# Optimization experiments

Measured on AMD Instinct MI355X. Metric: run time of the kernel, lower is better.

The kernel has to match this reference:

```python
import jax, jax.numpy as jnp
import numpy as np

# model dims (match init_kwargs)
D = 1024      # input_dim
H = 4096      # hidden_dim
O = 1024      # expert_output_dim
E = 8         # num_experts
K = 2         # top_k


def setup_inputs() -> dict:
    key = jax.random.key(0)
    ks = jax.random.split(key, 8)
    B, S = 2, 2048
    x = jax.random.normal(ks[0], (B, S, D), dtype=jnp.float32)
    s = 0.02
    Wr = jax.random.normal(ks[1], (D, E), dtype=jnp.float32) * s
    br = jnp.zeros((E,), dtype=jnp.float32)
    W1 = jax.random.normal(ks[2], (E, D, H), dtype=jnp.float32) * s
    b1 = jnp.zeros((E, H), dtype=jnp.float32)
    W2 = jax.random.normal(ks[3], (E, H, O), dtype=jnp.float32) * s
    b2 = jnp.zeros((E, O), dtype=jnp.float32)
    return {"x": x, "Wr": Wr, "br": br, "W1": W1, "b1": b1, "W2": W2, "b2": b2}


def reference(x, Wr, br, W1, b1, W2, b2):
    B, S, _ = x.shape
    T = B * S
    xf = x.reshape(T, D)                                  # [T, D]
    logits = xf @ Wr + br                                 # [T, E]
    topk_logits, topk_idx = jax.lax.top_k(logits, K)      # [T, K]
    gates = jax.nn.softmax(topk_logits, axis=1)           # softmax over the K selected logits
    # scatter gates into a dense [T, E] matrix (top-k indices are unique per token)
    dense_gates = jnp.zeros((T, E), dtype=logits.dtype).at[
        jnp.arange(T)[:, None], topk_idx
    ].set(gates)
    # run every expert FFN densely, then combine with (mostly-zero) gates
    h = jax.nn.relu(jnp.einsum('td,edh->teh', xf, W1) + b1)   # [T, E, H]
    y = jnp.einsum('teh,eho->teo', h, W2) + b2                # [T, E, O]
    out = jnp.einsum('te,teo->to', dense_gates, y)            # [T, O]
    return out.reshape(B, S, O)
```

## Files before the change

### kernel.cpp

```cpp
#include <hip/hip_runtime.h>
#include <stdint.h>

#define KD 1024
#define KH 4096
#define KO 1024
#define KE 8
#define KT 4096

typedef unsigned short u16;
typedef __bf16 bf16x8 __attribute__((ext_vector_type(8)));
typedef unsigned short ushort8 __attribute__((ext_vector_type(8)));
typedef float floatx4 __attribute__((ext_vector_type(4)));

__device__ __forceinline__ u16 f2bf(float f) {
  unsigned u = __float_as_uint(f);
  u += 0x7fffu + ((u >> 16) & 1u);
  return (u16)(u >> 16);
}

__device__ __forceinline__ void glds16(const u16* g, u16* l) {
  __builtin_amdgcn_global_load_lds(
      (const __attribute__((address_space(1))) unsigned int*)(g),
      (__attribute__((address_space(3))) unsigned int*)(l), 16, 0, 0);
}

#define WAITV8 asm volatile("s_waitcnt vmcnt(8)" ::: "memory")
#define WAITV0 asm volatile("s_waitcnt vmcnt(0)" ::: "memory")
#define WAITLG asm volatile("s_waitcnt lgkmcnt(0)" ::: "memory")
#define BAR    __builtin_amdgcn_s_barrier()

__global__ void cvt_x_k(const float* __restrict__ x, u16* __restrict__ xbf) {
  int i = blockIdx.x * blockDim.x + threadIdx.x;
  float4 v = ((const float4*)x)[i];
  union { u16 u[4]; uint2 v2; } o;
  o.u[0] = f2bf(v.x); o.u[1] = f2bf(v.y); o.u[2] = f2bf(v.z); o.u[3] = f2bf(v.w);
  ((uint2*)xbf)[i] = o.v2;
}

__global__ __launch_bounds__(256) void transpose_k(const float* __restrict__ in,
                                                   u16* __restrict__ out, int R, int C) {
  __shared__ float tile[64][65];
  const int e = blockIdx.z;
  const float* I = in + (size_t)e * R * C;
  u16* Oo = out + (size_t)e * R * C;
  const int c0 = blockIdx.x * 64, r0 = blockIdx.y * 64;
  const int t = threadIdx.x;
  const int rr = t >> 4;
  const int c4 = (t & 15) << 2;
#pragma unroll
  for (int j = 0; j < 4; j++) {
    int r = rr + j * 16;
    float4 v = *(const float4*)&I[(size_t)(r0 + r) * C + c0 + c4];
    tile[r][c4] = v.x; tile[r][c4 + 1] = v.y; tile[r][c4 + 2] = v.z; tile[r][c4 + 3] = v.w;
  }
  __syncthreads();
  const int cc = t >> 3;
  const int rb = (t & 7) << 3;
#pragma unroll
  for (int j = 0; j < 2; j++) {
    int c = cc + j * 32;
    ushort8 o;
#pragma unroll
    for (int k = 0; k < 8; k++) o[k] = f2bf(tile[rb + k][c]);
    *(ushort8*)&Oo[(size_t)(c0 + c) * R + r0 + rb] = o;
  }
}

__global__ void router_k(const float* __restrict__ x, const float* __restrict__ Wr,
                         const float* __restrict__ br, int* __restrict__ eidx,
                         float2* __restrict__ gpair) {
  const int t = blockIdx.x;
  const int lane = threadIdx.x;
  const float* xr = x + (size_t)t * KD;
  double acc[KE];
#pragma unroll
  for (int e = 0; e < KE; e++) acc[e] = 0.0;
  for (int i = lane; i < KD; i += 64) {
    float xv = xr[i];
    const float* wr = Wr + i * KE;
#pragma unroll
    for (int e = 0; e < KE; e++) acc[e] += (double)xv * (double)wr[e];
  }
#pragma unroll
  for (int e = 0; e < KE; e++) {
#pragma unroll
    for (int m = 32; m > 0; m >>= 1) acc[e] += __shfl_xor(acc[e], m, 64);
  }
  if (lane == 0) {
    float l[KE];
#pragma unroll
    for (int e = 0; e < KE; e++) l[e] = (float)acc[e] + br[e];
    int i0 = 0;
#pragma unroll
    for (int e = 1; e < KE; e++) if (l[e] > l[i0]) i0 = e;
    int i1 = -1;
#pragma unroll
    for (int e = 0; e < KE; e++) {
      if (e == i0) continue;
      if (i1 < 0 || l[e] > l[i1]) i1 = e;
    }
    float g0 = 1.0f / (1.0f + expf(l[i1] - l[i0]));
    eidx[t] = i0 | (i1 << 4);
    gpair[t] = make_float2(g0, 1.0f - g0);
  }
}

__global__ __launch_bounds__(256) void bucket_k(const int* __restrict__ eidx,
                                                int* __restrict__ cnt,
                                                int* __restrict__ tok,
                                                int* __restrict__ pos) {
  const int e = blockIdx.x;
  const int tid = threadIdx.x;
  const int t0 = tid * 16;
  int f[16]; int c = 0;
#pragma unroll
  for (int j = 0; j < 16; j++) {
    int pk = eidx[t0 + j];
    int h0 = ((pk & 15) == e);
    int h1 = (((pk >> 4) & 15) == e);
    f[j] = h0 ? 1 : (h1 ? 2 : 0);
    c += (f[j] != 0);
  }
  __shared__ int sc[256];
  sc[tid] = c;
  __syncthreads();
  for (int d = 1; d < 256; d <<= 1) {
    int add = (tid >= d) ? sc[tid - d] : 0;
    __syncthreads();
    sc[tid] += add;
    __syncthreads();
  }
  int base = sc[tid] - c;
  if (tid == 0) cnt[e] = sc[255];
#pragma unroll
  for (int j = 0; j < 16; j++) {
    if (f[j]) {
      tok[(e << 12) + base] = t0 + j;
      pos[2 * (t0 + j) + (f[j] - 1)] = base;
      base++;
    }
  }
}

__global__ void offsets_k(const int* __restrict__ cnt, int* __restrict__ offs) {
  if (threadIdx.x == 0 && blockIdx.x == 0) {
    int s = 0;
#pragma unroll
    for (int e = 0; e < KE; e++) { offs[e] = s; s += cnt[e]; }
  }
}

__global__ __launch_bounds__(256) void gemm1_k(
    const u16* __restrict__ xbf, const u16* __restrict__ w1t,
    const float* __restrict__ b1, const int* __restrict__ cnt,
    const int* __restrict__ offs, const int* __restrict__ tok,
    u16* __restrict__ hbuf) {
  const int e = blockIdx.z;
  const int me = cnt[e];
  const int m0 = blockIdx.y * 128;
  if (m0 >= me) return;
  const int n0 = blockIdx.x * 128;
  const int oe = offs[e];
  const int* tk = tok + (e << 12);

  __shared__ u16 As[2 * 8192];
  __shared__ u16 Bs[2 * 8192];

  const int tid = threadIdx.x;
  const int lane = tid & 63;
  const int w = tid >> 6;
  const int wm = w >> 1, wn = w & 1;

  const int rr = lane >> 2;
  const int cc = (lane & 3) << 3;
  const int ar0 = m0 + w * 32 + rr;
  const int ar1 = ar0 + 16;
  const int ta0 = (ar0 < me) ? tk[ar0] : 0;
  const int ta1 = (ar1 < me) ? tk[ar1] : 0;
  const u16* ga0 = xbf + ((size_t)ta0 << 10) + cc;
  const u16* ga1 = xbf + ((size_t)ta1 << 10) + cc;
  const int br0 = n0 + w * 32 + rr;
  const u16* gb0 = w1t + ((size_t)e << 22) + ((size_t)br0 << 10) + cc;
  const u16* gb1 = gb0 + (16 << 10);
  u16* la00 = &As[w * 1024] + lane * 8;
  u16* lb00 = &Bs[w * 1024] + lane * 8;

  floatx4 acc[4][4] = {};
  const int fr = lane & 15;
  const int kq = (lane >> 4) << 3;

  auto stage = [&](int k64, int off) {
    glds16(ga0 + k64,      la00 + off);
    glds16(ga1 + k64,      la00 + off + 512);
    glds16(ga0 + k64 + 32, la00 + off + 4096);
    glds16(ga1 + k64 + 32, la00 + off + 4096 + 512);
    glds16(gb0 + k64,      lb00 + off);
    glds16(gb1 + k64,      lb00 + off + 512);
    glds16(gb0 + k64 + 32, lb00 + off + 4096);
    glds16(gb1 + k64 + 32, lb00 + off + 4096 + 512);
  };
  auto compute = [&](int off) {
#pragma unroll
    for (int p = 0; p < 2; p++) {
      bf16x8 af[4], bfr[4];
#pragma unroll
      for (int i = 0; i < 4; i++) {
        af[i]  = __builtin_bit_cast(bf16x8, *(const ushort8*)&As[off + p * 4096 + (wm * 64 + i * 16 + fr) * 32 + kq]);
        bfr[i] = __builtin_bit_cast(bf16x8, *(const ushort8*)&Bs[off + p * 4096 + (wn * 64 + i * 16 + fr) * 32 + kq]);
      }
#pragma unroll
      for (int mi = 0; mi < 4; mi++)
#pragma unroll
        for (int ni = 0; ni < 4; ni++)
          acc[mi][ni] = __builtin_amdgcn_mfma_f32_16x16x32_bf16(af[mi], bfr[ni], acc[mi][ni], 0, 0, 0);
    }
  };

  stage(0, 0);
  stage(64, 8192);
  for (int kt = 0; kt < KD / 64 - 2; kt += 2) {
    WAITV8; BAR; compute(0);    WAITLG; BAR; stage((kt + 2) * 64, 0);
    WAITV8; BAR; compute(8192); WAITLG; BAR; stage((kt + 3) * 64, 8192);
  }
  WAITV8; BAR; compute(0);
  WAITV0; BAR; compute(8192);

  const int q = lane >> 4;
#pragma unroll
  for (int ni = 0; ni < 4; ni++) {
    const int gcol = n0 + wn * 64 + ni * 16 + fr;
    const float bb = b1[(e << 12) + gcol];
#pragma unroll
    for (int mi = 0; mi < 4; mi++) {
#pragma unroll
      for (int r = 0; r < 4; r++) {
        const int gr = m0 + wm * 64 + mi * 16 + q * 4 + r;
        if (gr < me) {
          float v = fmaxf(acc[mi][ni][r] + bb, 0.0f);
          hbuf[((size_t)(oe + gr) << 12) + gcol] = f2bf(v);
        }
      }
    }
  }
}

__global__ __launch_bounds__(256) void gemm2_k(
    const u16* __restrict__ hbuf, const u16* __restrict__ w2t,
    const int* __restrict__ cnt, const int* __restrict__ offs,
    float* __restrict__ y) {
  const int e = blockIdx.z;
  const int me = cnt[e];
  const int m0 = blockIdx.y * 128;
  if (m0 >= me) return;
  const int ks = blockIdx.x & 1;
  const int n0 = (blockIdx.x >> 1) * 128;
  const int k0 = ks * (KH / 2);
  const int oe = offs[e];

  __shared__ u16 As[2 * 8192];
  __shared__ u16 Bs[2 * 8192];

  const int tid = threadIdx.x;
  const int lane = tid & 63;
  const int w = tid >> 6;
  const int wm = w >> 1, wn = w & 1;

  const int rr = lane >> 2;
  const int cc = (lane & 3) << 3;
  const int ar0 = m0 + w * 32 + rr;
  const int ar1 = ar0 + 16;
  const int sl0 = oe + ((ar0 < me) ? ar0 : 0);
  const int sl1 = oe + ((ar1 < me) ? ar1 : 0);
  const u16* ga0 = hbuf + ((size_t)sl0 << 12) + k0 + cc;
  const u16* ga1 = hbuf + ((size_t)sl1 << 12) + k0 + cc;
  const int br0 = n0 + w * 32 + rr;
  const u16* gb0 = w2t + ((size_t)e << 22) + ((size_t)br0 << 12) + k0 + cc;
  const u16* gb1 = gb0 + (16 << 12);
  u16* la00 = &As[w * 1024] + lane * 8;
  u16* lb00 = &Bs[w * 1024] + lane * 8;

  floatx4 acc[4][4] = {};
  const int fr = lane & 15;
  const int kq = (lane >> 4) << 3;

  auto stage = [&](int k64, int off) {
    glds16(ga0 + k64,      la00 + off);
    glds16(ga1 + k64,      la00 + off + 512);
    glds16(ga0 + k64 + 32, la00 + off + 4096);
    glds16(ga1 + k64 + 32, la00 + off + 4096 + 512);
    glds16(gb0 + k64,      lb00 + off);
    glds16(gb1 + k64,      lb00 + off + 512);
    glds16(gb0 + k64 + 32, lb00 + off + 4096);
    glds16(gb1 + k64 + 32, lb00 + off + 4096 + 512);
  };
  auto compute = [&](int off) {
#pragma unroll
    for (int p = 0; p < 2; p++) {
      bf16x8 af[4], bfr[4];
#pragma unroll
      for (int i = 0; i < 4; i++) {
        af[i]  = __builtin_bit_cast(bf16x8, *(const ushort8*)&As[off + p * 4096 + (wm * 64 + i * 16 + fr) * 32 + kq]);
        bfr[i] = __builtin_bit_cast(bf16x8, *(const ushort8*)&Bs[off + p * 4096 + (wn * 64 + i * 16 + fr) * 32 + kq]);
      }
#pragma unroll
      for (int mi = 0; mi < 4; mi++)
#pragma unroll
        for (int ni = 0; ni < 4; ni++)
          acc[mi][ni] = __builtin_amdgcn_mfma_f32_16x16x32_bf16(af[mi], bfr[ni], acc[mi][ni], 0, 0, 0);
    }
  };

  stage(0, 0);
  stage(64, 8192);
  for (int kt = 0; kt < KH / 2 / 64 - 2; kt += 2) {
    WAITV8; BAR; compute(0);    WAITLG; BAR; stage((kt + 2) * 64, 0);
    WAITV8; BAR; compute(8192); WAITLG; BAR; stage((kt + 3) * 64, 8192);
  }
  WAITV8; BAR; compute(0);
  WAITV0; BAR; compute(8192);

  const int q = lane >> 4;
  float* yk = y + ((size_t)ks << 23);
#pragma unroll
  for (int mi = 0; mi < 4; mi++) {
#pragma unroll
    for (int r = 0; r < 4; r++) {
      const int gr = m0 + wm * 64 + mi * 16 + q * 4 + r;
      if (gr < me) {
        float* yrow = yk + ((size_t)(oe + gr) << 10);
#pragma unroll
        for (int ni = 0; ni < 4; ni++)
          yrow[n0 + wn * 64 + ni * 16 + fr] = acc[mi][ni][r];
      }
    }
  }
}

__global__ __launch_bounds__(256) void combine_k(
    const float* __restrict__ y, const int* __restrict__ eidx,
    const float2* __restrict__ gp, const int* __restrict__ offs,
    const int* __restrict__ pos, const float* __restrict__ b2,
    float* __restrict__ out) {
  const int t = blockIdx.x;
  const int c4 = threadIdx.x << 2;
  const int pk = eidx[t];
  const int e0 = pk & 15, e1 = (pk >> 4) & 15;
  const float2 g = gp[t];
  const int s0 = offs[e0] + pos[2 * t];
  const int s1 = offs[e1] + pos[2 * t + 1];
  float4 a0 = *(const float4*)(y + ((size_t)s0 << 10) + c4);
  float4 a1 = *(const float4*)(y + (1ull << 23) + ((size_t)s0 << 10) + c4);
  float4 c0 = *(const float4*)(y + ((size_t)s1 << 10) + c4);
  float4 c1 = *(const float4*)(y + (1ull << 23) + ((size_t)s1 << 10) + c4);
  float4 ba = *(const float4*)(b2 + (e0 << 10) + c4);
  float4 bc = *(const float4*)(b2 + (e1 << 10) + c4);
  float4 o;
  o.x = g.x * (a0.x + a1.x + ba.x) + g.y * (c0.x + c1.x + bc.x);
  o.y = g.x * (a0.y + a1.y + ba.y) + g.y * (c0.y + c1.y + bc.y);
  o.z = g.x * (a0.z + a1.z + ba.z) + g.y * (c0.z + c1.z + bc.z);
  o.w = g.x * (a0.w + a1.w + ba.w) + g.y * (c0.w + c1.w + bc.w);
  *(float4*)(out + ((size_t)t << 10) + c4) = o;
}

extern "C" void kernel_launch(void* const* d_in, const int* in_sizes, int n_in,
                              void* d_out, int out_size, void* d_ws, size_t ws_size,
                              hipStream_t stream) {
  const float* x  = (const float*)d_in[0];
  const float* Wr = (const float*)d_in[1];
  const float* br = (const float*)d_in[2];
  const float* W1 = (const float*)d_in[3];
  const float* b1 = (const float*)d_in[4];
  const float* W2 = (const float*)d_in[5];
  const float* b2 = (const float*)d_in[6];
  float* out = (float*)d_out;

  char* ws = (char*)d_ws;
  size_t p = 0;
  auto alloc = [&](size_t bytes) {
    void* r = ws + p;
    p = (p + bytes + 255) & ~(size_t)255;
    return r;
  };
  int*    cnt   = (int*)alloc(KE * 4);
  int*    offs  = (int*)alloc(KE * 4);
  int*    eidx  = (int*)alloc((size_t)KT * 4);
  float2* gpair = (float2*)alloc((size_t)KT * 8);
  int*    pos   = (int*)alloc((size_t)2 * KT * 4);
  int*    tok   = (int*)alloc((size_t)KE * KT * 4);
  u16*    xbf   = (u16*)alloc((size_t)KT * KD * 2);
  u16*    w1t   = (u16*)alloc((size_t)KE * KD * KH * 2);
  u16*    w2t   = (u16*)alloc((size_t)KE * KH * KO * 2);
  u16*    hbuf  = (u16*)alloc((size_t)2 * KT * KH * 2);
  float*  y     = (float*)w1t;

  cvt_x_k<<<(KT * KD / 4) / 256, 256, 0, stream>>>(x, xbf);
  transpose_k<<<dim3(KH / 64, KD / 64, KE), 256, 0, stream>>>(W1, w1t, KD, KH);
  transpose_k<<<dim3(KO / 64, KH / 64, KE), 256, 0, stream>>>(W2, w2t, KH, KO);
  router_k<<<KT, 64, 0, stream>>>(x, Wr, br, eidx, gpair);
  bucket_k<<<KE, 256, 0, stream>>>(eidx, cnt, tok, pos);
  offsets_k<<<1, 64, 0, stream>>>(cnt, offs);
  gemm1_k<<<dim3(KH / 128, KT / 128, KE), 256, 0, stream>>>(xbf, w1t, b1, cnt, offs, tok, hbuf);
  gemm2_k<<<dim3(2 * KO / 128, KT / 128, KE), 256, 0, stream>>>(hbuf, w2t, cnt, offs, y);
  combine_k<<<KT, 256, 0, stream>>>(y, eidx, gpair, offs, pos, b2, out);
}
```

Measured before the change: 614.6 us.

## Enlarge expert GEMM tiles to 256x256 with 8 waves and 4-stage pipeline

Both expert GEMMs move from 128x128 tiles with 4 waves and a two-buffer K=64 pipeline to 256x256 tiles with 8 waves. The new pipeline has four LDS stages of K=32, a single barrier pair per step and finer vmcnt waits, and raises wave priority around the MFMA block. The aim is more operand reuse per tile loaded from global memory and better hiding of load latency. In exchange it uses double the accumulator registers and 128KB of LDS per block, launches fewer blocks, and wastes more work on partially filled expert row tiles.

```diff
diff --git a/kernel.cpp b/kernel.cpp
--- a/kernel.cpp
+++ b/kernel.cpp
@@ -24,10 +24,8 @@
       (__attribute__((address_space(3))) unsigned int*)(l), 16, 0, 0);
 }
 
-#define WAITV8 asm volatile("s_waitcnt vmcnt(8)" ::: "memory")
-#define WAITV0 asm volatile("s_waitcnt vmcnt(0)" ::: "memory")
-#define WAITLG asm volatile("s_waitcnt lgkmcnt(0)" ::: "memory")
-#define BAR    __builtin_amdgcn_s_barrier()
+#define BAR __builtin_amdgcn_s_barrier()
+#define SB0 __builtin_amdgcn_sched_barrier(0)
 
 __global__ void cvt_x_k(const float* __restrict__ x, u16* __restrict__ xbf) {
   int i = blockIdx.x * blockDim.x + threadIdx.x;
@@ -150,91 +148,96 @@
   }
 }
 
-__global__ __launch_bounds__(256) void gemm1_k(
+__global__ __launch_bounds__(512, 2) void gemm1_k(
     const u16* __restrict__ xbf, const u16* __restrict__ w1t,
     const float* __restrict__ b1, const int* __restrict__ cnt,
     const int* __restrict__ offs, const int* __restrict__ tok,
     u16* __restrict__ hbuf) {
   const int e = blockIdx.z;
   const int me = cnt[e];
-  const int m0 = blockIdx.y * 128;
+  const int m0 = blockIdx.y * 256;
   if (m0 >= me) return;
-  const int n0 = blockIdx.x * 128;
+  const int n0 = blockIdx.x * 256;
   const int oe = offs[e];
   const int* tk = tok + (e << 12);
 
-  __shared__ u16 As[2 * 8192];
-  __shared__ u16 Bs[2 * 8192];
+  __shared__ u16 As[4 * 8192];
+  __shared__ u16 Bs[4 * 8192];
 
   const int tid = threadIdx.x;
   const int lane = tid & 63;
   const int w = tid >> 6;
-  const int wm = w >> 1, wn = w & 1;
-
-  const int rr = lane >> 2;
-  const int cc = (lane & 3) << 3;
-  const int ar0 = m0 + w * 32 + rr;
-  const int ar1 = ar0 + 16;
-  const int ta0 = (ar0 < me) ? tk[ar0] : 0;
-  const int ta1 = (ar1 < me) ? tk[ar1] : 0;
-  const u16* ga0 = xbf + ((size_t)ta0 << 10) + cc;
-  const u16* ga1 = xbf + ((size_t)ta1 << 10) + cc;
-  const int br0 = n0 + w * 32 + rr;
-  const u16* gb0 = w1t + ((size_t)e << 22) + ((size_t)br0 << 10) + cc;
-  const u16* gb1 = gb0 + (16 << 10);
-  u16* la00 = &As[w * 1024] + lane * 8;
-  u16* lb00 = &Bs[w * 1024] + lane * 8;
-
-  floatx4 acc[4][4] = {};
+  const int wm = w >> 2, wn = w & 3;
+
+  const int srow = w * 32 + (lane >> 2);
+  const int scol = (lane & 3) << 3;
+  const int gr0 = m0 + srow, gr1 = gr0 + 16;
+  const int ta0 = (gr0 < me) ? tk[gr0] : 0;
+  const int ta1 = (gr1 < me) ? tk[gr1] : 0;
+  const u16* gA0 = xbf + ((size_t)ta0 << 10) + scol;
+  const u16* gA1 = xbf + ((size_t)ta1 << 10) + scol;
+  const u16* gB0 = w1t + ((size_t)e << 22) + ((size_t)(n0 + srow) << 10) + scol;
+  const u16* gB1 = gB0 + (16 << 10);
+  u16* lA0 = As + w * 1024 + lane * 8;
+  u16* lB0 = Bs + w * 1024 + lane * 8;
+
+  floatx4 acc[8][4] = {};
   const int fr = lane & 15;
-  const int kq = (lane >> 4) << 3;
-
-  auto stage = [&](int k64, int off) {
-    glds16(ga0 + k64,      la00 + off);
-    glds16(ga1 + k64,      la00 + off + 512);
-    glds16(ga0 + k64 + 32, la00 + off + 4096);
-    glds16(ga1 + k64 + 32, la00 + off + 4096 + 512);
-    glds16(gb0 + k64,      lb00 + off);
-    glds16(gb1 + k64,      lb00 + off + 512);
-    glds16(gb0 + k64 + 32, lb00 + off + 4096);
-    glds16(gb1 + k64 + 32, lb00 + off + 4096 + 512);
+  const int q  = lane >> 4;
+  const int aoff = (wm * 128 + fr) * 32 + q * 8;
+  const int boff = (wn * 64  + fr) * 32 + q * 8;
+
+  auto stage = [&](int t) {
+    const int buf = (t & 3) * 8192;
+    const int k = t * 32;
+    glds16(gA0 + k, lA0 + buf);
+    glds16(gA1 + k, lA0 + buf + 512);
+    glds16(gB0 + k, lB0 + buf);
+    glds16(gB1 + k, lB0 + buf + 512);
   };
-  auto compute = [&](int off) {
-#pragma unroll
-    for (int p = 0; p < 2; p++) {
-      bf16x8 af[4], bfr[4];
-#pragma unroll
-      for (int i = 0; i < 4; i++) {
-        af[i]  = __builtin_bit_cast(bf16x8, *(const ushort8*)&As[off + p * 4096 + (wm * 64 + i * 16 + fr) * 32 + kq]);
-        bfr[i] = __builtin_bit_cast(bf16x8, *(const ushort8*)&Bs[off + p * 4096 + (wn * 64 + i * 16 + fr) * 32 + kq]);
-      }
-#pragma unroll
-      for (int mi = 0; mi < 4; mi++)
-#pragma unroll
-        for (int ni = 0; ni < 4; ni++)
-          acc[mi][ni] = __builtin_amdgcn_mfma_f32_16x16x32_bf16(af[mi], bfr[ni], acc[mi][ni], 0, 0, 0);
-    }
+  auto compute = [&](int t) {
+    const int buf = (t & 3) * 8192;
+    __builtin_amdgcn_s_setprio(1);
+    bf16x8 a[8], b[4];
+#pragma unroll
+    for (int ni = 0; ni < 4; ni++)
+      b[ni] = __builtin_bit_cast(bf16x8, *(const ushort8*)&Bs[buf + boff + ni * 512]);
+#pragma unroll
+    for (int mi = 0; mi < 8; mi++)
+      a[mi] = __builtin_bit_cast(bf16x8, *(const ushort8*)&As[buf + aoff + mi * 512]);
+#pragma unroll
+    for (int mi = 0; mi < 8; mi++)
+#pragma unroll
+      for (int ni = 0; ni < 4; ni++)
+        acc[mi][ni] = __builtin_amdgcn_mfma_f32_16x16x32_bf16(a[mi], b[ni], acc[mi][ni], 0, 0, 0);
+    __builtin_amdgcn_s_setprio(0);
   };
 
-  stage(0, 0);
-  stage(64, 8192);
-  for (int kt = 0; kt < KD / 64 - 2; kt += 2) {
-    WAITV8; BAR; compute(0);    WAITLG; BAR; stage((kt + 2) * 64, 0);
-    WAITV8; BAR; compute(8192); WAITLG; BAR; stage((kt + 3) * 64, 8192);
-  }
-  WAITV8; BAR; compute(0);
-  WAITV0; BAR; compute(8192);
-
-  const int q = lane >> 4;
+  const int NT = KD / 32;
+  stage(0); stage(1); stage(2);
+  for (int t = 0; t < NT - 3; ++t) {
+    stage(t + 3);
+    asm volatile("s_waitcnt vmcnt(12)" ::: "memory");
+    BAR; SB0;
+    compute(t);
+    SB0; BAR;
+  }
+  asm volatile("s_waitcnt vmcnt(8)" ::: "memory");
+  BAR; SB0; compute(NT - 3); SB0; BAR;
+  asm volatile("s_waitcnt vmcnt(4)" ::: "memory");
+  BAR; SB0; compute(NT - 2); SB0; BAR;
+  asm volatile("s_waitcnt vmcnt(0)" ::: "memory");
+  BAR; SB0; compute(NT - 1);
+
 #pragma unroll
   for (int ni = 0; ni < 4; ni++) {
     const int gcol = n0 + wn * 64 + ni * 16 + fr;
     const float bb = b1[(e << 12) + gcol];
 #pragma unroll
-    for (int mi = 0; mi < 4; mi++) {
+    for (int mi = 0; mi < 8; mi++) {
 #pragma unroll
       for (int r = 0; r < 4; r++) {
-        const int gr = m0 + wm * 64 + mi * 16 + q * 4 + r;
+        const int gr = m0 + wm * 128 + mi * 16 + q * 4 + r;
         if (gr < me) {
           float v = fmaxf(acc[mi][ni][r] + bb, 0.0f);
           hbuf[((size_t)(oe + gr) << 12) + gcol] = f2bf(v);
@@ -244,88 +247,93 @@
   }
 }
 
-__global__ __launch_bounds__(256) void gemm2_k(
+__global__ __launch_bounds__(512, 2) void gemm2_k(
     const u16* __restrict__ hbuf, const u16* __restrict__ w2t,
     const int* __restrict__ cnt, const int* __restrict__ offs,
     float* __restrict__ y) {
   const int e = blockIdx.z;
   const int me = cnt[e];
-  const int m0 = blockIdx.y * 128;
+  const int m0 = blockIdx.y * 256;
   if (m0 >= me) return;
   const int ks = blockIdx.x & 1;
-  const int n0 = (blockIdx.x >> 1) * 128;
+  const int n0 = (blockIdx.x >> 1) * 256;
   const int k0 = ks * (KH / 2);
   const int oe = offs[e];
 
-  __shared__ u16 As[2 * 8192];
-  __shared__ u16 Bs[2 * 8192];
+  __shared__ u16 As[4 * 8192];
+  __shared__ u16 Bs[4 * 8192];
 
   const int tid = threadIdx.x;
   const int lane = tid & 63;
   const int w = tid >> 6;
-  const int wm = w >> 1, wn = w & 1;
-
-  const int rr = lane >> 2;
-  const int cc = (lane & 3) << 3;
-  const int ar0 = m0 + w * 32 + rr;
-  const int ar1 = ar0 + 16;
+  const int wm = w >> 2, wn = w & 3;
+
+  const int srow = w * 32 + (lane >> 2);
+  const int scol = (lane & 3) << 3;
+  const int ar0 = m0 + srow, ar1 = ar0 + 16;
   const int sl0 = oe + ((ar0 < me) ? ar0 : 0);
   const int sl1 = oe + ((ar1 < me) ? ar1 : 0);
-  const u16* ga0 = hbuf + ((size_t)sl0 << 12) + k0 + cc;
-  const u16* ga1 = hbuf + ((size_t)sl1 << 12) + k0 + cc;
-  const int br0 = n0 + w * 32 + rr;
-  const u16* gb0 = w2t + ((size_t)e << 22) + ((size_t)br0 << 12) + k0 + cc;
-  const u16* gb1 = gb0 + (16 << 12);
-  u16* la00 = &As[w * 1024] + lane * 8;
-  u16* lb00 = &Bs[w * 1024] + lane * 8;
-
-  floatx4 acc[4][4] = {};
+  const u16* gA0 = hbuf + ((size_t)sl0 << 12) + k0 + scol;
+  const u16* gA1 = hbuf + ((size_t)sl1 << 12) + k0 + scol;
+  const u16* gB0 = w2t + ((size_t)e << 22) + ((size_t)(n0 + srow) << 12) + k0 + scol;
+  const u16* gB1 = gB0 + (16 << 12);
+  u16* lA0 = As + w * 1024 + lane * 8;
+  u16* lB0 = Bs + w * 1024 + lane * 8;
+
+  floatx4 acc[8][4] = {};
   const int fr = lane & 15;
-  const int kq = (lane >> 4) << 3;
-
-  auto stage = [&](int k64, int off) {
-    glds16(ga0 + k64,      la00 + off);
-    glds16(ga1 + k64,      la00 + off + 512);
-    glds16(ga0 + k64 + 32, la00 + off + 4096);
-    glds16(ga1 + k64 + 32, la00 + off + 4096 + 512);
-    glds16(gb0 + k64,      lb00 + off);
-    glds16(gb1 + k64,      lb00 + off + 512);
-    glds16(gb0 + k64 + 32, lb00 + off + 4096);
-    glds16(gb1 + k64 + 32, lb00 + off + 4096 + 512);
+  const int q  = lane >> 4;
+  const int aoff = (wm * 128 + fr) * 32 + q * 8;
+  const int boff = (wn * 64  + fr) * 32 + q * 8;
+
+  auto stage = [&](int t) {
+    const int buf = (t & 3) * 8192;
+    const int k = t * 32;
+    glds16(gA0 + k, lA0 + buf);
+    glds16(gA1 + k, lA0 + buf + 512);
+    glds16(gB0 + k, lB0 + buf);
+    glds16(gB1 + k, lB0 + buf + 512);
   };
-  auto compute = [&](int off) {
-#pragma unroll
-    for (int p = 0; p < 2; p++) {
-      bf16x8 af[4], bfr[4];
-#pragma unroll
-      for (int i = 0; i < 4; i++) {
-        af[i]  = __builtin_bit_cast(bf16x8, *(const ushort8*)&As[off + p * 4096 + (wm * 64 + i * 16 + fr) * 32 + kq]);
-        bfr[i] = __builtin_bit_cast(bf16x8, *(const ushort8*)&Bs[off + p * 4096 + (wn * 64 + i * 16 + fr) * 32 + kq]);
-      }
-#pragma unroll
-      for (int mi = 0; mi < 4; mi++)
-#pragma unroll
-        for (int ni = 0; ni < 4; ni++)
-          acc[mi][ni] = __builtin_amdgcn_mfma_f32_16x16x32_bf16(af[mi], bfr[ni], acc[mi][ni], 0, 0, 0);
-    }
+  auto compute = [&](int t) {
+    const int buf = (t & 3) * 8192;
+    __builtin_amdgcn_s_setprio(1);
+    bf16x8 a[8], b[4];
+#pragma unroll
+    for (int ni = 0; ni < 4; ni++)
+      b[ni] = __builtin_bit_cast(bf16x8, *(const ushort8*)&Bs[buf + boff + ni * 512]);
+#pragma unroll
+    for (int mi = 0; mi < 8; mi++)
+      a[mi] = __builtin_bit_cast(bf16x8, *(const ushort8*)&As[buf + aoff + mi * 512]);
+#pragma unroll
+    for (int mi = 0; mi < 8; mi++)
+#pragma unroll
+      for (int ni = 0; ni < 4; ni++)
+        acc[mi][ni] = __builtin_amdgcn_mfma_f32_16x16x32_bf16(a[mi], b[ni], acc[mi][ni], 0, 0, 0);
+    __builtin_amdgcn_s_setprio(0);
   };
 
-  stage(0, 0);
-  stage(64, 8192);
-  for (int kt = 0; kt < KH / 2 / 64 - 2; kt += 2) {
-    WAITV8; BAR; compute(0);    WAITLG; BAR; stage((kt + 2) * 64, 0);
-    WAITV8; BAR; compute(8192); WAITLG; BAR; stage((kt + 3) * 64, 8192);
-  }
-  WAITV8; BAR; compute(0);
-  WAITV0; BAR; compute(8192);
-
-  const int q = lane >> 4;
+  const int NT = (KH / 2) / 32;
+  stage(0); stage(1); stage(2);
+  for (int t = 0; t < NT - 3; ++t) {
+    stage(t + 3);
+    asm volatile("s_waitcnt vmcnt(12)" ::: "memory");
+    BAR; SB0;
+    compute(t);
+    SB0; BAR;
+  }
+  asm volatile("s_waitcnt vmcnt(8)" ::: "memory");
+  BAR; SB0; compute(NT - 3); SB0; BAR;
+  asm volatile("s_waitcnt vmcnt(4)" ::: "memory");
+  BAR; SB0; compute(NT - 2); SB0; BAR;
+  asm volatile("s_waitcnt vmcnt(0)" ::: "memory");
+  BAR; SB0; compute(NT - 1);
+
   float* yk = y + ((size_t)ks << 23);
 #pragma unroll
-  for (int mi = 0; mi < 4; mi++) {
+  for (int mi = 0; mi < 8; mi++) {
 #pragma unroll
     for (int r = 0; r < 4; r++) {
-      const int gr = m0 + wm * 64 + mi * 16 + q * 4 + r;
+      const int gr = m0 + wm * 128 + mi * 16 + q * 4 + r;
       if (gr < me) {
         float* yrow = yk + ((size_t)(oe + gr) << 10);
 #pragma unroll
@@ -399,7 +407,7 @@
   router_k<<<KT, 64, 0, stream>>>(x, Wr, br, eidx, gpair);
   bucket_k<<<KE, 256, 0, stream>>>(eidx, cnt, tok, pos);
   offsets_k<<<1, 64, 0, stream>>>(cnt, offs);
-  gemm1_k<<<dim3(KH / 128, KT / 128, KE), 256, 0, stream>>>(xbf, w1t, b1, cnt, offs, tok, hbuf);
-  gemm2_k<<<dim3(2 * KO / 128, KT / 128, KE), 256, 0, stream>>>(hbuf, w2t, cnt, offs, y);
+  gemm1_k<<<dim3(KH / 256, KT / 256, KE), 512, 0, stream>>>(xbf, w1t, b1, cnt, offs, tok, hbuf);
+  gemm2_k<<<dim3(2 * KO / 256, KT / 256, KE), 512, 0, stream>>>(hbuf, w2t, cnt, offs, y);
   combine_k<<<KT, 256, 0, stream>>>(y, eidx, gpair, offs, pos, b2, out);
 }
```

New measurement: 673.4 us. 9.6% more time.
